# Kernel optimization log

Hardware: AMD Instinct MI355X
Metric: run time of the kernel (lower is better)

Reference implementation:

```python
import jax, jax.numpy as jnp
import numpy as np

EMB_DIM, NUM_LEVELS, NUM_HEADS, NUM_POINTS = 256, 4, 8, 4
LEVEL_SHAPES = np.array([[128, 128], [64, 64], [32, 32], [16, 16]], dtype=np.int64)
B, N_Q = 8, 900
N_IMG = int((LEVEL_SHAPES[:, 0] * LEVEL_SHAPES[:, 1]).sum())  # 21760


def _offset_bias():
    # Faithful to the torch init: per-head square pattern scaled by point index.
    H, L, P = NUM_HEADS, NUM_LEVELS, NUM_POINTS
    angles = jnp.linspace(0.0, 2.0 * np.pi * (H - 1) / H, H)
    circle = jnp.stack([jnp.sin(angles), jnp.cos(angles)], axis=-1)          # [H,2]
    square = circle / jnp.max(jnp.abs(circle), axis=-1, keepdims=True)       # [H,2]
    squares = jnp.tile(square[:, None, None, :], (1, L, P, 1))               # [H,L,P,2]
    squares = squares * jnp.arange(1, P + 1, dtype=jnp.float32)[:, None]
    return squares.reshape(-1).astype(jnp.float32)


def setup_inputs() -> dict:
    key = jax.random.key(0)
    ks = jax.random.split(key, 12)
    C = EMB_DIM
    H, L, P = NUM_HEADS, NUM_LEVELS, NUM_POINTS
    s = 0.02
    return {
        'query_feat': jax.random.normal(ks[0], (B, N_Q, C), jnp.float32),
        'query_points': jax.random.uniform(ks[1], (B, N_Q, 4), jnp.float32, 0.1, 0.9),
        'img_feat': jax.random.normal(ks[2], (B, N_IMG, C), jnp.float32),
        'img_valid_ratios': jnp.ones((B, L, 2), jnp.float32),
        'img_mask': jnp.zeros((B, N_IMG), bool),
        'img_shapes': jnp.asarray(LEVEL_SHAPES),
        'W_img': jax.random.normal(ks[3], (C, C), jnp.float32) * s,
        'b_img': jax.random.normal(ks[4], (C,), jnp.float32) * s,
        'W_off': jax.random.normal(ks[5], (C, H * L * P * 2), jnp.float32) * 0.001,
        'b_off': _offset_bias(),
        'W_attn': jax.random.normal(ks[6], (C, H * L * P), jnp.float32) * s,
        'b_attn': jax.random.normal(ks[7], (H * L * P,), jnp.float32) * s,
        'W_out': jax.random.normal(ks[8], (C, C), jnp.float32) * s,
        'b_out': jax.random.normal(ks[9], (C,), jnp.float32) * s,
    }


def _bilinear_sample(value, loc, Hl, Wl):
    # value: [B,Hh,Hl*Wl,d]; loc: [B,Hh,Q,P,2] (x,y) normalized to [0,1]
    # grid_sample bilinear, padding_mode='zeros', align_corners=False
    Bb, Hh = value.shape[0], value.shape[1]
    x = loc[..., 0] * Wl - 0.5
    y = loc[..., 1] * Hl - 0.5
    x0f = jnp.floor(x); y0f = jnp.floor(y)
    wx = x - x0f; wy = y - y0f
    x0 = x0f.astype(jnp.int32); y0 = y0f.astype(jnp.int32)

    def gather(yi, xi):
        valid = (yi >= 0) & (yi < Hl) & (xi >= 0) & (xi < Wl)
        idx = jnp.clip(yi, 0, Hl - 1) * Wl + jnp.clip(xi, 0, Wl - 1)
        flat = idx.reshape(Bb, Hh, -1)[..., None]                 # [B,Hh,Q*P,1]
        g = jnp.take_along_axis(value, flat, axis=2)              # [B,Hh,Q*P,d]
        g = g.reshape(*idx.shape, value.shape[-1])                # [B,Hh,Q,P,d]
        return g * valid[..., None]

    v00 = gather(y0, x0); v01 = gather(y0, x0 + 1)
    v10 = gather(y0 + 1, x0); v11 = gather(y0 + 1, x0 + 1)
    w00 = ((1 - wy) * (1 - wx))[..., None]; w01 = ((1 - wy) * wx)[..., None]
    w10 = (wy * (1 - wx))[..., None]; w11 = (wy * wx)[..., None]
    return v00 * w00 + v01 * w01 + v10 * w10 + v11 * w11


def _msda(img_feat, img_shapes, sampling_points, attention_weights):
    # img_feat [B,N,Hh,d]; sampling_points [B,Q,Hh,L,P,2]; attn [B,Q,Hh,L,P]
    shapes = np.asarray(img_shapes)  # static level metadata
    Bb, N, Hh, d = img_feat.shape
    Q = sampling_points.shape[1]
    value = jnp.transpose(img_feat, (0, 2, 1, 3))                     # [B,Hh,N,d]
    loc = jnp.transpose(sampling_points, (0, 2, 1, 3, 4, 5))          # [B,Hh,Q,L,P,2]
    attn = jnp.transpose(attention_weights, (0, 2, 1, 3, 4))          # [B,Hh,Q,L,P]
    out = jnp.zeros((Bb, Hh, Q, d), img_feat.dtype)
    start = 0
    for l in range(shapes.shape[0]):
        Hl, Wl = int(shapes[l, 0]), int(shapes[l, 1])
        v = value[:, :, start:start + Hl * Wl]
        s = _bilinear_sample(v, loc[:, :, :, l], Hl, Wl)              # [B,Hh,Q,P,d]
        out = out + jnp.einsum('bhqpd,bhqp->bhqd', s, attn[:, :, :, l])
        start += Hl * Wl
    return jnp.transpose(out, (0, 2, 1, 3)).reshape(Bb, Q, Hh * d)


def reference(query_feat, query_points, img_feat, img_valid_ratios, img_mask,
              img_shapes, W_img, b_img, W_off, b_off, W_attn, b_attn, W_out, b_out):
    Bb, N_img, C = img_feat.shape
    N_q = query_feat.shape[1]
    Hh, L, P = NUM_HEADS, NUM_LEVELS, NUM_POINTS
    v = img_feat @ W_img + b_img
    v = jnp.where(img_mask[..., None], 0.0, v).reshape(Bb, N_img, Hh, C // Hh)
    offs = (query_feat @ W_off + b_off).reshape(Bb, N_q, Hh, L, P, 2)
    attn = jax.nn.softmax((query_feat @ W_attn + b_attn).reshape(Bb, N_q, Hh, L * P), axis=-1)
    attn = attn.reshape(Bb, N_q, Hh, L, P)
    # box branch (query_points last dim == 4), cxcywh relative coords
    vr = jnp.tile(img_valid_ratios[..., ::-1], (1, 1, 2))             # [B,L,4]
    qp = query_points[:, :, None, :] * vr[:, None, :, :]              # [B,Nq,L,4]
    sp = qp[:, :, None, :, None, :2] + offs * qp[:, :, None, :, None, 2:] / (2.0 * P)
    out = _msda(v, img_shapes, sp, attn)                              # [B,Nq,C]
    return out @ W_out + b_out
```

## Files before the change

kernel.cpp:

```cpp
#include <hip/hip_runtime.h>

#define NQ 900
#define NIMG 21760

typedef __attribute__((ext_vector_type(8))) short short8v;
typedef __attribute__((ext_vector_type(4))) float f32x4;
typedef unsigned short ushort_t;

__device__ __forceinline__ void split_bf16(float a, ushort_t& hi, ushort_t& lo) {
  unsigned u = __float_as_uint(a);
  unsigned hu = u & 0xFFFF0000u;
  hi = (ushort_t)(hu >> 16);
  float lf = a - __uint_as_float(hu);
  unsigned lu = __float_as_uint(lf);
  unsigned r = lu + 0x7FFFu + ((lu >> 16) & 1u);
  lo = (ushort_t)(r >> 16);
}

__device__ __forceinline__ ushort_t f32_to_bf16_rne(float a) {
  unsigned u = __float_as_uint(a);
  unsigned r = u + 0x7FFFu + ((u >> 16) & 1u);
  return (ushort_t)(r >> 16);
}

union U8v {
  unsigned u[4];
  short8v v;
};

__device__ __forceinline__ short8v cvt8(float4 x, float4 y) {
  U8v r;
  asm("v_cvt_pk_bf16_f32 %0, %1, %2" : "=v"(r.u[0]) : "v"(x.x), "v"(x.y));
  asm("v_cvt_pk_bf16_f32 %0, %1, %2" : "=v"(r.u[1]) : "v"(x.z), "v"(x.w));
  asm("v_cvt_pk_bf16_f32 %0, %1, %2" : "=v"(r.u[2]) : "v"(y.x), "v"(y.y));
  asm("v_cvt_pk_bf16_f32 %0, %1, %2" : "=v"(r.u[3]) : "v"(y.z), "v"(y.w));
  return r.v;
}

__device__ __forceinline__ void split8(float4 x, float4 y, short8v& h, short8v& l) {
  float xf[8] = {x.x, x.y, x.z, x.w, y.x, y.y, y.z, y.w};
  U8v H, L;
#pragma unroll
  for (int i = 0; i < 4; ++i) {
    const unsigned u0 = __float_as_uint(xf[2 * i]);
    const unsigned u1 = __float_as_uint(xf[2 * i + 1]);
    H.u[i] = (u1 & 0xFFFF0000u) | (u0 >> 16);
    const float l0 = xf[2 * i] - __uint_as_float(u0 & 0xFFFF0000u);
    const float l1 = xf[2 * i + 1] - __uint_as_float(u1 & 0xFFFF0000u);
    L.u[i] = (__float_as_uint(l1) & 0xFFFF0000u) | (__float_as_uint(l0) >> 16);
  }
  h = H.v;
  l = L.v;
}

__global__ __launch_bounds__(256) void wprep_kernel(
    const float* __restrict__ Wimg, const float* __restrict__ Wout,
    ushort_t* __restrict__ Wh, ushort_t* __restrict__ Wh2,
    ushort_t* __restrict__ Wl2) {
  const int blk = blockIdx.x;
  const int idx = (blk & 255) * 256 + threadIdx.x;
  const int k = idx >> 8, col = idx & 255;
  if (blk < 256) {
    Wh[col * 256 + k] = f32_to_bf16_rne(Wimg[idx]);
  } else {
    ushort_t h, l;
    split_bf16(Wout[idx], h, l);
    Wh2[col * 256 + k] = h;
    Wl2[col * 256 + k] = l;
  }
}

#define NBLK 512
#define NTILES 5440
__global__ __launch_bounds__(256, 2) void vproj_persist(
    const float* __restrict__ A, const ushort_t* __restrict__ Wh,
    const float* __restrict__ bias, ushort_t* __restrict__ v) {
  __shared__ __align__(16) float Abuf[2][32 * 256];

  const int t = threadIdx.x;
  const int w = t >> 6, lane = t & 63;
  const int lr = lane & 15, lg = lane >> 4;

  short8v bB[8][4];
#pragma unroll
  for (int ks = 0; ks < 8; ++ks)
#pragma unroll
    for (int n = 0; n < 4; ++n) {
      const int col = w * 64 + n * 16 + lr;
      bB[ks][n] = *(const short8v*)(Wh + (size_t)col * 256 + ks * 32 + lg * 8);
    }
  float bcol[4];
#pragma unroll
  for (int n = 0; n < 4; ++n) bcol[n] = bias[w * 64 + n * 16 + lr];

  auto STAGE = [&](int buf, int tile) {
#pragma unroll
    for (int j = 0; j < 8; ++j) {
      const int ob = j * 4096 + w * 1024;
      const int o = ob + lane * 16;
      const int r = o >> 10;
      const int ir = (o & 1023) ^ ((r & 7) << 4);
      const float* gp = A + (size_t)(tile * 32 + r) * 256 + (ir >> 2);
      char* lp = (char*)(&Abuf[buf][0]) + ob;
      __builtin_amdgcn_global_load_lds(
          (const __attribute__((address_space(1))) void*)gp,
          (__attribute__((address_space(3))) void*)lp, 16, 0, 0);
    }
  };

  int tile = blockIdx.x;
  STAGE(0, tile);
  int cur = 0;

  for (; tile < NTILES; tile += NBLK) {
    const int nxt = tile + NBLK;
    if (nxt < NTILES) {
      STAGE(cur ^ 1, nxt);
      asm volatile("s_waitcnt vmcnt(8)" ::: "memory");
    } else {
      asm volatile("s_waitcnt vmcnt(0)" ::: "memory");
    }
    __builtin_amdgcn_s_barrier();
    __builtin_amdgcn_sched_barrier(0);

    f32x4 acc[2][4];
#pragma unroll
    for (int m = 0; m < 2; ++m)
#pragma unroll
      for (int n = 0; n < 4; ++n) {
        acc[m][n][0] = 0.f; acc[m][n][1] = 0.f;
        acc[m][n][2] = 0.f; acc[m][n][3] = 0.f;
      }

    const char* AB = (const char*)&Abuf[cur][0];
#pragma unroll
    for (int ks = 0; ks < 8; ++ks) {
      short8v ah[2];
#pragma unroll
      for (int m = 0; m < 2; ++m) {
        const int row = m * 16 + lr;
        const int a0 = row * 1024 + ((ks * 128 + lg * 32) ^ ((row & 7) << 4));
        const float4 x = *(const float4*)(AB + a0);
        const float4 y = *(const float4*)(AB + (a0 ^ 16));
        ah[m] = cvt8(x, y);
      }
#pragma unroll
      for (int n = 0; n < 4; ++n)
#pragma unroll
        for (int m = 0; m < 2; ++m)
          acc[m][n] = __builtin_amdgcn_mfma_f32_16x16x32_bf16(ah[m], bB[ks][n], acc[m][n], 0, 0, 0);
    }
    __builtin_amdgcn_sched_barrier(0);

    const int bb = tile / 680;
    const int pix0 = (tile - bb * 680) * 32;
    ushort_t* vbase = v + ((size_t)bb * 8 * NIMG + pix0) * 32;
#pragma unroll
    for (int n = 0; n < 4; ++n) {
      const int col = w * 64 + n * 16 + lr;
      const int h = col >> 5, ch = col & 31;
      ushort_t* vh = vbase + (size_t)h * (NIMG * 32) + ch;
#pragma unroll
      for (int m = 0; m < 2; ++m) {
        const int prow = m * 16 + lg * 4;
#pragma unroll
        for (int j = 0; j < 4; ++j)
          vh[(prow + j) * 32] = f32_to_bf16_rne(acc[m][n][j] + bcol[n]);
      }
    }
    __builtin_amdgcn_s_barrier();
    cur ^= 1;
  }
}

__global__ __launch_bounds__(256) void gemm_noLds(
    const float* __restrict__ A, const ushort_t* __restrict__ Wh,
    const ushort_t* __restrict__ Wl, const float* __restrict__ bias,
    float* __restrict__ C, int M) {
  const int t = threadIdx.x;
  const int colblk = blockIdx.x & 3;
  const int rowblk = blockIdx.x >> 2;
  const int col0 = colblk * 64;

  const int lane = t & 63, w = t >> 6;
  const int lr = lane & 15, lg = lane >> 4;
  const int wrow0 = rowblk * 64 + w * 16;

  f32x4 acc[4];
#pragma unroll
  for (int n = 0; n < 4; ++n) {
    acc[n][0] = 0.f; acc[n][1] = 0.f; acc[n][2] = 0.f; acc[n][3] = 0.f;
  }

#pragma unroll
  for (int ks = 0; ks < 8; ++ks) {
    int row = wrow0 + lr;
    row = min(row, M - 1);
    const float4* ap = (const float4*)(A + (size_t)row * 256 + ks * 32 + lg * 8);
    short8v ah, al;
    split8(ap[0], ap[1], ah, al);
    const int k0 = ks * 32 + lg * 8;
#pragma unroll
    for (int n = 0; n < 4; ++n) {
      const int col = col0 + n * 16 + lr;
      const short8v bh = *(const short8v*)(Wh + col * 256 + k0);
      const short8v bl = *(const short8v*)(Wl + col * 256 + k0);
      acc[n] = __builtin_amdgcn_mfma_f32_16x16x32_bf16(ah, bh, acc[n], 0, 0, 0);
      acc[n] = __builtin_amdgcn_mfma_f32_16x16x32_bf16(ah, bl, acc[n], 0, 0, 0);
      acc[n] = __builtin_amdgcn_mfma_f32_16x16x32_bf16(al, bh, acc[n], 0, 0, 0);
    }
  }

#pragma unroll
  for (int n = 0; n < 4; ++n) {
    const int col = col0 + n * 16 + lr;
    const float b = bias[col];
#pragma unroll
    for (int j = 0; j < 4; ++j) {
      const int row = wrow0 + lg * 4 + j;
      if (row < M) C[(size_t)row * 256 + col] = acc[n][j] + b;
    }
  }
}

__global__ __launch_bounds__(384) void qproj_kernel(
    const float* __restrict__ qf, const float* __restrict__ qpts_g,
    const float* __restrict__ ivr, const float* __restrict__ Woff,
    const float* __restrict__ boff, const float* __restrict__ Wattn,
    const float* __restrict__ battn, float* __restrict__ sp,
    float* __restrict__ attn) {
  __shared__ __align__(16) float qlds[8 * 256];
  __shared__ float qp[8][4];
  __shared__ float vr[8][8];
  __shared__ float logits[8][128];
  const int t = threadIdx.x;
  const int row0 = blockIdx.x * 8;

  for (int idx = t; idx < 8 * 256; idx += 384)
    qlds[idx] = qf[(size_t)row0 * 256 + idx];
  if (t < 32) {
    const int m = t >> 2, j = t & 3;
    qp[m][j] = qpts_g[(size_t)(row0 + m) * 4 + j];
  }
  if (t >= 32 && t < 96) {
    const int u = t - 32;
    const int m = u >> 3, j = u & 7;
    const int b = (row0 + m) / NQ;
    vr[m][j] = ivr[b * 8 + j];
  }
  __syncthreads();

  float acc[8];
#pragma unroll
  for (int m = 0; m < 8; ++m) acc[m] = 0.f;

  const float4* q4 = (const float4*)qlds;
  const int c = t - 256;
  for (int k4 = 0; k4 < 64; ++k4) {
    float w0, w1, w2, w3;
    if (t < 256) {
      w0 = Woff[(k4 * 4 + 0) * 256 + t];
      w1 = Woff[(k4 * 4 + 1) * 256 + t];
      w2 = Woff[(k4 * 4 + 2) * 256 + t];
      w3 = Woff[(k4 * 4 + 3) * 256 + t];
    } else {
      w0 = Wattn[(k4 * 4 + 0) * 128 + c];
      w1 = Wattn[(k4 * 4 + 1) * 128 + c];
      w2 = Wattn[(k4 * 4 + 2) * 128 + c];
      w3 = Wattn[(k4 * 4 + 3) * 128 + c];
    }
#pragma unroll
    for (int m = 0; m < 8; ++m) {
      const float4 f = q4[m * 64 + k4];
      acc[m] = fmaf(f.x, w0, acc[m]);
      acc[m] = fmaf(f.y, w1, acc[m]);
      acc[m] = fmaf(f.z, w2, acc[m]);
      acc[m] = fmaf(f.w, w3, acc[m]);
    }
  }

  if (t >= 256) {
    const float bb = battn[c];
#pragma unroll
    for (int m = 0; m < 8; ++m) logits[m][c] = acc[m] + bb;
  }
  __syncthreads();

  if (t < 64) {
    const int m = t >> 3, h = t & 7;
    float mx = -1e30f;
#pragma unroll
    for (int j = 0; j < 16; ++j) mx = fmaxf(mx, logits[m][h * 16 + j]);
    float e[16];
    float s = 0.f;
#pragma unroll
    for (int j = 0; j < 16; ++j) {
      e[j] = expf(logits[m][h * 16 + j] - mx);
      s += e[j];
    }
    const float inv = 1.f / s;
    const size_t row = row0 + m;
#pragma unroll
    for (int j = 0; j < 16; ++j) attn[row * 128 + h * 16 + j] = e[j] * inv;
  }

  if (t < 256) {
    const int xy = t & 1;
    const int l = (t >> 3) & 3;
    const float bo = boff[t];
#pragma unroll
    for (int m = 0; m < 8; ++m) {
      const float val = acc[m] + bo;
      const float r = vr[m][l * 2 + (xy ^ 1)];
      const float ctr = qp[m][xy] * r;
      const float scl = qp[m][2 + xy] * r * 0.125f;
      sp[(size_t)(row0 + m) * 256 + t] = ctr + val * scl;
    }
  }
}

__global__ __launch_bounds__(256) void msda_kernel(
    const ushort_t* __restrict__ v, const float* __restrict__ sp,
    const float* __restrict__ attn, float* __restrict__ outk) {
  __shared__ __align__(16) float splds[1024];
  __shared__ __align__(16) float alds[512];
  __shared__ int ioff[16 * 2 * 32];
  __shared__ float wgt[16 * 4 * 32];
  const int t = threadIdx.x;
  const int bid = (int)(blockIdx.x & 7) * 225 + (int)(blockIdx.x >> 3);
  const int row0 = bid * 4;

  ((float4*)splds)[t] = ((const float4*)(sp + (size_t)row0 * 256))[t];
  if (t < 128)
    ((float4*)alds)[t] = ((const float4*)(attn + (size_t)row0 * 128))[t];
  __syncthreads();

#pragma unroll
  for (int it = 0; it < 2; ++it) {
    const int s = it * 256 + t;
    const int q = s >> 7, h = (s >> 4) & 7, l = (s >> 2) & 3, p = s & 3;
    const int un = q * 8 + h;
    const int j = l * 4 + p;
    const float spx = splds[q * 256 + h * 32 + l * 8 + p * 2];
    const float spy = splds[q * 256 + h * 32 + l * 8 + p * 2 + 1];
    const float a = alds[q * 128 + h * 16 + l * 4 + p];
    const int WL = 128 >> l;
    const int start = (65536 - (65536 >> (2 * l))) / 3;
    const float x = spx * (float)WL - 0.5f;
    const float y = spy * (float)WL - 0.5f;
    const float x0f = floorf(x), y0f = floorf(y);
    const float wx = x - x0f, wy = y - y0f;
    const int x0 = (int)x0f, y0 = (int)y0f;
    const int x1 = x0 + 1, y1 = y0 + 1;
    const int bx = min(max(x0, 0), WL - 2);
    const bool vx0 = (x0 >= 0) & (x0 < WL), vx1 = (x1 >= 0) & (x1 < WL);
    float wxl = 0.f, wxr = 0.f;
    if (vx0 & (x0 == bx)) wxl += 1.f - wx;
    if (vx1 & (x1 == bx)) wxl += wx;
    if (vx0 & (x0 == bx + 1)) wxr += 1.f - wx;
    if (vx1 & (x1 == bx + 1)) wxr += wx;
    const int cy0 = min(max(y0, 0), WL - 1), cy1 = min(max(y1, 0), WL - 1);
    const float ay0 = ((y0 >= 0) & (y0 < WL)) ? a * (1.f - wy) : 0.f;
    const float ay1 = ((y1 >= 0) & (y1 < WL)) ? a * wy : 0.f;
    ioff[(j * 2 + 0) * 32 + un] = (start + cy0 * WL + bx) * 32;
    ioff[(j * 2 + 1) * 32 + un] = (start + cy1 * WL + bx) * 32;
    wgt[(j * 4 + 0) * 32 + un] = ay0 * wxl;
    wgt[(j * 4 + 1) * 32 + un] = ay0 * wxr;
    wgt[(j * 4 + 2) * 32 + un] = ay1 * wxl;
    wgt[(j * 4 + 3) * 32 + un] = ay1 * wxr;
  }
  __syncthreads();

  const int q = t >> 6, h = (t >> 3) & 7, d8 = t & 7;
  const int un = q * 8 + h;
  const int cq = d8 & 3, half = d8 >> 2;
  const int row = row0 + q;
  const int b = row / NQ;
  const ushort_t* vbl =
      v + ((size_t)(b * 8 + h) * NIMG) * 32 + half * 32 + cq * 8;

  float acc[8];
#pragma unroll
  for (int i = 0; i < 8; ++i) acc[i] = 0.f;

#pragma unroll
  for (int j = 0; j < 16; ++j) {
#pragma unroll
    for (int r = 0; r < 2; ++r) {
      const int off = ioff[(j * 2 + r) * 32 + un];
      const float wc = wgt[(j * 4 + r * 2 + half) * 32 + un];
      const uint4 uu = *(const uint4*)(vbl + off);
      acc[0] = fmaf(wc, __uint_as_float(uu.x << 16), acc[0]);
      acc[1] = fmaf(wc, __uint_as_float(uu.x & 0xFFFF0000u), acc[1]);
      acc[2] = fmaf(wc, __uint_as_float(uu.y << 16), acc[2]);
      acc[3] = fmaf(wc, __uint_as_float(uu.y & 0xFFFF0000u), acc[3]);
      acc[4] = fmaf(wc, __uint_as_float(uu.z << 16), acc[4]);
      acc[5] = fmaf(wc, __uint_as_float(uu.z & 0xFFFF0000u), acc[5]);
      acc[6] = fmaf(wc, __uint_as_float(uu.w << 16), acc[6]);
      acc[7] = fmaf(wc, __uint_as_float(uu.w & 0xFFFF0000u), acc[7]);
    }
  }

#pragma unroll
  for (int i = 0; i < 8; ++i) acc[i] += __shfl_xor(acc[i], 4);

  float4 o;
  o.x = acc[half * 4 + 0];
  o.y = acc[half * 4 + 1];
  o.z = acc[half * 4 + 2];
  o.w = acc[half * 4 + 3];
  *(float4*)(outk + (size_t)row * 256 + h * 32 + cq * 8 + half * 4) = o;
}

extern "C" void kernel_launch(void* const* d_in, const int* in_sizes, int n_in,
                              void* d_out, int out_size, void* d_ws, size_t ws_size,
                              hipStream_t stream) {
  const float* query_feat   = (const float*)d_in[0];
  const float* query_points = (const float*)d_in[1];
  const float* img_feat     = (const float*)d_in[2];
  const float* ivr          = (const float*)d_in[3];
  const float* W_img  = (const float*)d_in[6];
  const float* b_img  = (const float*)d_in[7];
  const float* W_off  = (const float*)d_in[8];
  const float* b_off  = (const float*)d_in[9];
  const float* W_attn = (const float*)d_in[10];
  const float* b_attn = (const float*)d_in[11];
  const float* W_out  = (const float*)d_in[12];
  const float* b_out  = (const float*)d_in[13];
  float* out = (float*)d_out;

  float* ws   = (float*)d_ws;
  ushort_t* v = (ushort_t*)ws;
  float* sp   = (float*)(v + 44564480);
  float* attn = sp + 1843200;
  float* mso  = attn + 921600;
  ushort_t* Wh  = (ushort_t*)(mso + 1843200);
  ushort_t* Wh2 = Wh + 65536;
  ushort_t* Wl2 = Wh2 + 65536;

  wprep_kernel<<<512, 256, 0, stream>>>(W_img, W_out, Wh, Wh2, Wl2);
  vproj_persist<<<NBLK, 256, 0, stream>>>(img_feat, Wh, b_img, v);
  qproj_kernel<<<900, 384, 0, stream>>>(query_feat, query_points, ivr,
                                        W_off, b_off, W_attn, b_attn, sp, attn);
  msda_kernel<<<1800, 256, 0, stream>>>(v, sp, attn, mso);
  gemm_noLds<<<113 * 4, 256, 0, stream>>>(mso, Wh2, Wl2, b_out, out, 7200);
}
```

Baseline: 148.8 us.

## Use single bf16 output projection and relax vproj load waits with LDS prefetch

Replaces the split hi/lo bf16 three-MFMA output GEMM with a single bf16 MFMA per tile, dropping the low-part weight buffer and split arithmetic. In the persistent value-projection kernel, the vmcnt waits are loosened so later tiles do not wait on the global stores still in flight, and LDS reads are software-prefetched two k-steps ahead. This trades output-projection precision for fewer MFMAs and loads, and the relaxed waitcnt values depend on the exact count of outstanding memory operations.

```diff
diff --git a/kernel.cpp b/kernel.cpp
--- a/kernel.cpp
+++ b/kernel.cpp
@@ -6,16 +6,6 @@
 typedef __attribute__((ext_vector_type(8))) short short8v;
 typedef __attribute__((ext_vector_type(4))) float f32x4;
 typedef unsigned short ushort_t;
-
-__device__ __forceinline__ void split_bf16(float a, ushort_t& hi, ushort_t& lo) {
-  unsigned u = __float_as_uint(a);
-  unsigned hu = u & 0xFFFF0000u;
-  hi = (ushort_t)(hu >> 16);
-  float lf = a - __uint_as_float(hu);
-  unsigned lu = __float_as_uint(lf);
-  unsigned r = lu + 0x7FFFu + ((lu >> 16) & 1u);
-  lo = (ushort_t)(r >> 16);
-}
 
 __device__ __forceinline__ ushort_t f32_to_bf16_rne(float a) {
   unsigned u = __float_as_uint(a);
@@ -37,37 +27,16 @@
   return r.v;
 }
 
-__device__ __forceinline__ void split8(float4 x, float4 y, short8v& h, short8v& l) {
-  float xf[8] = {x.x, x.y, x.z, x.w, y.x, y.y, y.z, y.w};
-  U8v H, L;
-#pragma unroll
-  for (int i = 0; i < 4; ++i) {
-    const unsigned u0 = __float_as_uint(xf[2 * i]);
-    const unsigned u1 = __float_as_uint(xf[2 * i + 1]);
-    H.u[i] = (u1 & 0xFFFF0000u) | (u0 >> 16);
-    const float l0 = xf[2 * i] - __uint_as_float(u0 & 0xFFFF0000u);
-    const float l1 = xf[2 * i + 1] - __uint_as_float(u1 & 0xFFFF0000u);
-    L.u[i] = (__float_as_uint(l1) & 0xFFFF0000u) | (__float_as_uint(l0) >> 16);
-  }
-  h = H.v;
-  l = L.v;
-}
-
 __global__ __launch_bounds__(256) void wprep_kernel(
     const float* __restrict__ Wimg, const float* __restrict__ Wout,
-    ushort_t* __restrict__ Wh, ushort_t* __restrict__ Wh2,
-    ushort_t* __restrict__ Wl2) {
+    ushort_t* __restrict__ Wh, ushort_t* __restrict__ Wh2) {
   const int blk = blockIdx.x;
   const int idx = (blk & 255) * 256 + threadIdx.x;
   const int k = idx >> 8, col = idx & 255;
-  if (blk < 256) {
+  if (blk < 256)
     Wh[col * 256 + k] = f32_to_bf16_rne(Wimg[idx]);
-  } else {
-    ushort_t h, l;
-    split_bf16(Wout[idx], h, l);
-    Wh2[col * 256 + k] = h;
-    Wl2[col * 256 + k] = l;
-  }
+  else
+    Wh2[col * 256 + k] = f32_to_bf16_rne(Wout[idx]);
 }
 
 #define NBLK 512
@@ -116,9 +85,12 @@
     const int nxt = tile + NBLK;
     if (nxt < NTILES) {
       STAGE(cur ^ 1, nxt);
-      asm volatile("s_waitcnt vmcnt(8)" ::: "memory");
+      if (tile == (int)blockIdx.x)
+        asm volatile("s_waitcnt vmcnt(8)" ::: "memory");
+      else
+        asm volatile("s_waitcnt vmcnt(40)" ::: "memory");
     } else {
-      asm volatile("s_waitcnt vmcnt(0)" ::: "memory");
+      asm volatile("s_waitcnt vmcnt(32)" ::: "memory");
     }
     __builtin_amdgcn_s_barrier();
     __builtin_amdgcn_sched_barrier(0);
@@ -133,16 +105,32 @@
       }
 
     const char* AB = (const char*)&Abuf[cur][0];
+
+    float4 px[2][2], py[2][2];
+#pragma unroll
+    for (int p = 0; p < 2; ++p)
+#pragma unroll
+      for (int m = 0; m < 2; ++m) {
+        const int row = m * 16 + lr;
+        const int a0 = row * 1024 + ((p * 128 + lg * 32) ^ ((row & 7) << 4));
+        px[p][m] = *(const float4*)(AB + a0);
+        py[p][m] = *(const float4*)(AB + (a0 ^ 16));
+      }
+
 #pragma unroll
     for (int ks = 0; ks < 8; ++ks) {
       short8v ah[2];
 #pragma unroll
-      for (int m = 0; m < 2; ++m) {
-        const int row = m * 16 + lr;
-        const int a0 = row * 1024 + ((ks * 128 + lg * 32) ^ ((row & 7) << 4));
-        const float4 x = *(const float4*)(AB + a0);
-        const float4 y = *(const float4*)(AB + (a0 ^ 16));
-        ah[m] = cvt8(x, y);
+      for (int m = 0; m < 2; ++m) ah[m] = cvt8(px[ks & 1][m], py[ks & 1][m]);
+      if (ks < 6) {
+#pragma unroll
+        for (int m = 0; m < 2; ++m) {
+          const int row = m * 16 + lr;
+          const int a0 =
+              row * 1024 + (((ks + 2) * 128 + lg * 32) ^ ((row & 7) << 4));
+          px[ks & 1][m] = *(const float4*)(AB + a0);
+          py[ks & 1][m] = *(const float4*)(AB + (a0 ^ 16));
+        }
       }
 #pragma unroll
       for (int n = 0; n < 4; ++n)
@@ -175,8 +163,7 @@
 
 __global__ __launch_bounds__(256) void gemm_noLds(
     const float* __restrict__ A, const ushort_t* __restrict__ Wh,
-    const ushort_t* __restrict__ Wl, const float* __restrict__ bias,
-    float* __restrict__ C, int M) {
+    const float* __restrict__ bias, float* __restrict__ C, int M) {
   const int t = threadIdx.x;
   const int colblk = blockIdx.x & 3;
   const int rowblk = blockIdx.x >> 2;
@@ -197,17 +184,13 @@
     int row = wrow0 + lr;
     row = min(row, M - 1);
     const float4* ap = (const float4*)(A + (size_t)row * 256 + ks * 32 + lg * 8);
-    short8v ah, al;
-    split8(ap[0], ap[1], ah, al);
+    const short8v ah = cvt8(ap[0], ap[1]);
     const int k0 = ks * 32 + lg * 8;
 #pragma unroll
     for (int n = 0; n < 4; ++n) {
       const int col = col0 + n * 16 + lr;
       const short8v bh = *(const short8v*)(Wh + col * 256 + k0);
-      const short8v bl = *(const short8v*)(Wl + col * 256 + k0);
       acc[n] = __builtin_amdgcn_mfma_f32_16x16x32_bf16(ah, bh, acc[n], 0, 0, 0);
-      acc[n] = __builtin_amdgcn_mfma_f32_16x16x32_bf16(ah, bl, acc[n], 0, 0, 0);
-      acc[n] = __builtin_amdgcn_mfma_f32_16x16x32_bf16(al, bh, acc[n], 0, 0, 0);
     }
   }
 
@@ -436,12 +419,11 @@
   float* mso  = attn + 921600;
   ushort_t* Wh  = (ushort_t*)(mso + 1843200);
   ushort_t* Wh2 = Wh + 65536;
-  ushort_t* Wl2 = Wh2 + 65536;
-
-  wprep_kernel<<<512, 256, 0, stream>>>(W_img, W_out, Wh, Wh2, Wl2);
+
+  wprep_kernel<<<512, 256, 0, stream>>>(W_img, W_out, Wh, Wh2);
   vproj_persist<<<NBLK, 256, 0, stream>>>(img_feat, Wh, b_img, v);
   qproj_kernel<<<900, 384, 0, stream>>>(query_feat, query_points, ivr,
                                         W_off, b_off, W_attn, b_attn, sp, attn);
   msda_kernel<<<1800, 256, 0, stream>>>(v, sp, attn, mso);
-  gemm_noLds<<<113 * 4, 256, 0, stream>>>(mso, Wh2, Wl2, b_out, out, 7200);
-}
+  gemm_noLds<<<113 * 4, 256, 0, stream>>>(mso, Wh2, b_out, out, 7200);
+}
```

Result: faster. 142.3 us (-4.4%).
